# Performance work log

Measured on AMD Instinct MI355X. Metric: run time of the kernel, lower is better.

The kernel has to match this reference:

```python
import jax, jax.numpy as jnp
import numpy as np

D = 384      # ViT-S feature dim (feat_dim_lookup['s'])
H = 6        # module forces num_heads = 6
L = 12       # ViT-S depth
RATIO = 0.1  # attention_mask_ratio
EPS = 1e-6


def layernorm(x, g, b):
    m = x.mean(-1, keepdims=True)
    v = ((x - m) ** 2).mean(-1, keepdims=True)
    return (x - m) * jax.lax.rsqrt(v + EPS) * g + b


def masked_attn(x, w_qkv, b_qkv, w_o, b_o):
    # Patch._fix_attn_masking: full softmax attention, threshold at ratio*row_max, renormalize.
    B, N, Dm = x.shape
    dh = Dm // H
    qkv = (x @ w_qkv + b_qkv).reshape(B, N, 3, H, dh)
    q = qkv[:, :, 0].transpose(0, 2, 1, 3)  # [B,H,N,dh]
    k = qkv[:, :, 1].transpose(0, 2, 1, 3)
    v = qkv[:, :, 2].transpose(0, 2, 1, 3)
    scores = jnp.einsum('bhqd,bhkd->bhqk', q, k) * (dh ** -0.5)
    attn = jax.nn.softmax(scores, axis=-1)
    thresh = RATIO * attn.max(axis=-1, keepdims=True)
    attn = jnp.where(attn >= thresh, attn, 0.0)
    attn = attn / attn.sum(axis=-1, keepdims=True)  # re-normalize
    out = jnp.einsum('bhqk,bhkd->bhqd', attn, v)
    out = out.transpose(0, 2, 1, 3).reshape(B, N, Dm)
    return out @ w_o + b_o, attn


def block(x, p):
    w_qkv, b_qkv, w_o, b_o, g1, be1, g2, be2, w1, b1, w2, b2 = p
    h, attn = masked_attn(layernorm(x, g1, be1), w_qkv, b_qkv, w_o, b_o)
    x = x + h
    h = layernorm(x, g2, be2) @ w1 + b1
    h = jax.nn.gelu(h, approximate=False) @ w2 + b2
    return x + h, attn


def setup_inputs() -> dict:
    key = jax.random.key(0)
    ks = jax.random.split(key, 8)
    B, N = 2, 962  # 2 transforms; (1+(160-8)//5)**2 + 1 cls = 962 tokens
    s = 0.02
    return {
        'x': jax.random.normal(ks[0], (B, N, D), jnp.float32),
        'w_qkv': jax.random.normal(ks[1], (L, D, 3 * D), jnp.float32) * s,
        'b_qkv': jnp.zeros((L, 3 * D), jnp.float32),
        'w_proj': jax.random.normal(ks[2], (L, D, D), jnp.float32) * s,
        'b_proj': jnp.zeros((L, D), jnp.float32),
        'ln1_g': jnp.ones((L, D), jnp.float32),
        'ln1_b': jnp.zeros((L, D), jnp.float32),
        'ln2_g': jnp.ones((L, D), jnp.float32),
        'ln2_b': jnp.zeros((L, D), jnp.float32),
        'w_fc1': jax.random.normal(ks[3], (L, D, 4 * D), jnp.float32) * s,
        'b_fc1': jnp.zeros((L, 4 * D), jnp.float32),
        'w_fc2': jax.random.normal(ks[4], (L, 4 * D, D), jnp.float32) * s,
        'b_fc2': jnp.zeros((L, D), jnp.float32),
        'lnf_g': jnp.ones((D,), jnp.float32),
        'lnf_b': jnp.zeros((D,), jnp.float32),
    }


def reference(x, w_qkv, b_qkv, w_proj, b_proj, ln1_g, ln1_b, ln2_g, ln2_b,
              w_fc1, b_fc1, w_fc2, b_fc2, lnf_g, lnf_b):
    params = (w_qkv, b_qkv, w_proj, b_proj, ln1_g, ln1_b, ln2_g, ln2_b,
              w_fc1, b_fc1, w_fc2, b_fc2)
    first = jax.tree_util.tree_map(lambda a: a[:-1], params)
    last = jax.tree_util.tree_map(lambda a: a[-1], params)

    def scan_fn(h, p):
        h, _ = block(h, p)
        return h, None

    x, _ = jax.lax.scan(scan_fn, x, first)  # blocks 0..L-2
    x, attn = block(x, last)                # last block, keep masked attention
    feats = layernorm(x, lnf_g, lnf_b)      # [B, N, D]
    return feats, attn
```

## Files before the change

### kernel.cpp

```cpp
#include <hip/hip_runtime.h>
#include <hip/hip_bf16.h>
#include <math.h>

typedef __bf16 bf16_t;
typedef __bf16 bf16x8 __attribute__((ext_vector_type(8)));
typedef float f32x4 __attribute__((ext_vector_type(4)));
typedef float f32x16 __attribute__((ext_vector_type(16)));

#define NEGBIG -3.0e38f

__global__ void __launch_bounds__(256) trall_k(
    const float* __restrict__ w_qkv, const float* __restrict__ w_proj,
    const float* __restrict__ w_fc1, const float* __restrict__ w_fc2,
    bf16_t* __restrict__ wt_qkv, bf16_t* __restrict__ wt_proj,
    bf16_t* __restrict__ wt_fc1, bf16_t* __restrict__ wt_fc2)
{
    __shared__ float T[32][33];
    int t = blockIdx.x;
    int z = t / 1728, r = t % 1728;
    const float* W; bf16_t* Wt; int K, N, n0, k0;
    if (r < 432)       { W = w_qkv;  Wt = wt_qkv;  K = 384;  N = 1152; n0 = (r % 36) * 32;               k0 = (r / 36) * 32; }
    else if (r < 576)  { W = w_proj; Wt = wt_proj; K = 384;  N = 384;  int rr = r - 432;  n0 = (rr % 12) * 32; k0 = (rr / 12) * 32; }
    else if (r < 1152) { W = w_fc1;  Wt = wt_fc1;  K = 384;  N = 1536; int rr = r - 576;  n0 = (rr % 48) * 32; k0 = (rr / 48) * 32; }
    else               { W = w_fc2;  Wt = wt_fc2;  K = 1536; N = 384;  int rr = r - 1152; n0 = (rr % 12) * 32; k0 = (rr / 12) * 32; }
    const float* Wl = W + (size_t)z * K * N;
    bf16_t* Wtl = Wt + (size_t)z * K * N;
    int tx = threadIdx.x & 31, ty = threadIdx.x >> 5;
#pragma unroll
    for (int i = 0; i < 4; ++i)
        T[ty + 8 * i][tx] = Wl[(size_t)(k0 + ty + 8 * i) * N + n0 + tx];
    __syncthreads();
#pragma unroll
    for (int i = 0; i < 4; ++i)
        Wtl[(size_t)(n0 + ty + 8 * i) * K + k0 + tx] = (bf16_t)T[tx][ty + 8 * i];
}

__global__ void __launch_bounds__(256) lncopy_k(
    const float* __restrict__ xin, const float* __restrict__ g,
    const float* __restrict__ b, float* __restrict__ xf,
    bf16_t* __restrict__ out)
{
    int t = blockIdx.x * 4 + (threadIdx.x >> 6);
    int lane = threadIdx.x & 63;
    const float* xp = xin + (size_t)t * 384;
    float v[6];
    float s = 0.f;
#pragma unroll
    for (int i = 0; i < 6; ++i) { v[i] = xp[lane + 64 * i]; s += v[i]; }
#pragma unroll
    for (int i = 0; i < 6; ++i) xf[(size_t)t * 384 + lane + 64 * i] = v[i];
    for (int off = 32; off > 0; off >>= 1) s += __shfl_xor(s, off);
    float mean = s * (1.0f / 384.0f);
    float s2 = 0.f;
#pragma unroll
    for (int i = 0; i < 6; ++i) { float d = v[i] - mean; s2 += d * d; }
    for (int off = 32; off > 0; off >>= 1) s2 += __shfl_xor(s2, off);
    float rstd = rsqrtf(s2 * (1.0f / 384.0f) + 1e-6f);
#pragma unroll
    for (int i = 0; i < 6; ++i) {
        int c = lane + 64 * i;
        out[(size_t)t * 384 + c] = (bf16_t)((v[i] - mean) * rstd * g[c] + b[c]);
    }
}

template <int NP, typename OT, bool WX>
__global__ void __launch_bounds__(256) ln_red_k(
    const float* __restrict__ x, const float* __restrict__ part,
    const float* __restrict__ g, const float* __restrict__ b,
    float* __restrict__ xupd, OT* __restrict__ out)
{
    int t = blockIdx.x * 4 + (threadIdx.x >> 6);
    int lane = threadIdx.x & 63;
    const size_t base = (size_t)t * 384;
    float v[6];
#pragma unroll
    for (int i = 0; i < 6; ++i) v[i] = x[base + lane + 64 * i];
#pragma unroll
    for (int p = 0; p < NP; ++p)
#pragma unroll
        for (int i = 0; i < 6; ++i)
            v[i] += part[(size_t)p * 738816 + base + lane + 64 * i];
    float s = 0.f;
#pragma unroll
    for (int i = 0; i < 6; ++i) {
        if (WX) xupd[base + lane + 64 * i] = v[i];
        s += v[i];
    }
    for (int off = 32; off > 0; off >>= 1) s += __shfl_xor(s, off);
    float mean = s * (1.0f / 384.0f);
    float s2 = 0.f;
#pragma unroll
    for (int i = 0; i < 6; ++i) { float d = v[i] - mean; s2 += d * d; }
    for (int off = 32; off > 0; off >>= 1) s2 += __shfl_xor(s2, off);
    float rstd = rsqrtf(s2 * (1.0f / 384.0f) + 1e-6f);
#pragma unroll
    for (int i = 0; i < 6; ++i) {
        int c = lane + 64 * i;
        out[base + c] = (OT)((v[i] - mean) * rstd * g[c] + b[c]);
    }
}

template <int MODE>
__global__ void __launch_bounds__(256) gemm_k(
    const bf16_t* __restrict__ A, const bf16_t* __restrict__ Bt,
    const float* __restrict__ bias, int M, int N, int K,
    bf16_t* __restrict__ outb,
    bf16_t* __restrict__ qb, bf16_t* __restrict__ kb, bf16_t* __restrict__ vtb)
{
    __shared__ alignas(16) bf16_t As[2][64][72];
    __shared__ alignas(16) bf16_t Bs[2][64][72];

    const int tid  = threadIdx.x;
    const int wave = tid >> 6, lane = tid & 63;
    const int m0 = blockIdx.y * 64, n0 = blockIdx.x * 64;
    const int rb = (wave >> 1) * 32, cb = (wave & 1) * 32;
    const int r32 = lane & 31, half = lane >> 5;
    const int h8 = half * 8;

    const int lrow = tid >> 3;
    const int lcol = (tid & 7) * 8;

    const bf16_t* pA0 = A  + (size_t)(m0 + lrow) * K + lcol;
    const bf16_t* pA1 = pA0 + (size_t)32 * K;
    const bf16_t* pB0 = Bt + (size_t)(n0 + lrow) * K + lcol;
    const bf16_t* pB1 = pB0 + (size_t)32 * K;

    f32x16 acc = {};
    bf16x8 va0, va1, vb0, vb1;

    va0 = *(const bf16x8*)(pA0);
    va1 = *(const bf16x8*)(pA1);
    vb0 = *(const bf16x8*)(pB0);
    vb1 = *(const bf16x8*)(pB1);
    *(bf16x8*)(&As[0][lrow][lcol])      = va0;
    *(bf16x8*)(&As[0][lrow + 32][lcol]) = va1;
    *(bf16x8*)(&Bs[0][lrow][lcol])      = vb0;
    *(bf16x8*)(&Bs[0][lrow + 32][lcol]) = vb1;

    int cur = 0;
    for (int k0 = 0; k0 < K; k0 += 64) {
        __syncthreads();
        const bool has_next = (k0 + 64 < K);
        if (has_next) {
            va0 = *(const bf16x8*)(pA0 + k0 + 64);
            va1 = *(const bf16x8*)(pA1 + k0 + 64);
            vb0 = *(const bf16x8*)(pB0 + k0 + 64);
            vb1 = *(const bf16x8*)(pB1 + k0 + 64);
        }
#pragma unroll
        for (int kc = 0; kc < 64; kc += 16) {
            bf16x8 a = *(const bf16x8*)(&As[cur][rb + r32][kc + h8]);
            bf16x8 b = *(const bf16x8*)(&Bs[cur][cb + r32][kc + h8]);
            acc = __builtin_amdgcn_mfma_f32_32x32x16_bf16(a, b, acc, 0, 0, 0);
        }
        if (has_next) {
            int nxt = cur ^ 1;
            *(bf16x8*)(&As[nxt][lrow][lcol])      = va0;
            *(bf16x8*)(&As[nxt][lrow + 32][lcol]) = va1;
            *(bf16x8*)(&Bs[nxt][lrow][lcol])      = vb0;
            *(bf16x8*)(&Bs[nxt][lrow + 32][lcol]) = vb1;
            cur = nxt;
        }
    }

    const int gc = n0 + cb + r32;
    const float bv = bias[gc];
    if (MODE == 2) {
#pragma unroll
        for (int reg = 0; reg < 16; ++reg) {
            int gr = m0 + rb + (reg & 3) + 8 * (reg >> 2) + 4 * half;
            if (gr >= M) continue;
            float val = acc[reg] + bv;
            float g = 0.5f * val * (1.0f + erff(val * 0.70710678118654752f));
            outb[(size_t)gr * N + gc] = (bf16_t)g;
        }
    } else {
        const int which = gc / 384, rem = gc % 384;
        const int h = rem >> 6, d = rem & 63;
#pragma unroll
        for (int reg = 0; reg < 16; ++reg) {
            int gr = m0 + rb + (reg & 3) + 8 * (reg >> 2) + 4 * half;
            if (gr >= M) continue;
            float val = acc[reg] + bv;
            int bb = (gr >= 962) ? 1 : 0;
            int n = gr - 962 * bb;
            int bh = bb * 6 + h;
            bf16_t bvv = (bf16_t)val;
            if (which == 0)      qb[((size_t)bh * 962 + n) * 64 + d] = bvv;
            else if (which == 1) kb[((size_t)bh * 962 + n) * 64 + d] = bvv;
            else                 vtb[((size_t)bh * 64 + d) * 992 + n] = bvv;
        }
    }
}

template <int KLEN>
__global__ void __launch_bounds__(256) gemm_sp(
    const bf16_t* __restrict__ A, int lda,
    const bf16_t* __restrict__ Bt, int ldb,
    const float* __restrict__ bias, int M, int N,
    float* __restrict__ part)
{
    __shared__ alignas(16) bf16_t As[2][64][72];
    __shared__ alignas(16) bf16_t Bs[2][64][72];

    const int tid  = threadIdx.x;
    const int wave = tid >> 6, lane = tid & 63;
    const int m0 = blockIdx.y * 64, n0 = blockIdx.x * 64;
    const int rb = (wave >> 1) * 32, cb = (wave & 1) * 32;
    const int r32 = lane & 31, half = lane >> 5;
    const int h8 = half * 8;
    const int ks = blockIdx.z * KLEN;

    const int lrow = tid >> 3;
    const int lcol = (tid & 7) * 8;

    const bf16_t* pA0 = A  + (size_t)(m0 + lrow) * lda + ks + lcol;
    const bf16_t* pA1 = pA0 + (size_t)32 * lda;
    const bf16_t* pB0 = Bt + (size_t)(n0 + lrow) * ldb + ks + lcol;
    const bf16_t* pB1 = pB0 + (size_t)32 * ldb;

    f32x16 acc = {};
    bf16x8 va0, va1, vb0, vb1;

    va0 = *(const bf16x8*)(pA0);
    va1 = *(const bf16x8*)(pA1);
    vb0 = *(const bf16x8*)(pB0);
    vb1 = *(const bf16x8*)(pB1);
    *(bf16x8*)(&As[0][lrow][lcol])      = va0;
    *(bf16x8*)(&As[0][lrow + 32][lcol]) = va1;
    *(bf16x8*)(&Bs[0][lrow][lcol])      = vb0;
    *(bf16x8*)(&Bs[0][lrow + 32][lcol]) = vb1;

    int cur = 0;
    for (int k0 = 0; k0 < KLEN; k0 += 64) {
        __syncthreads();
        const bool has_next = (k0 + 64 < KLEN);
        if (has_next) {
            va0 = *(const bf16x8*)(pA0 + k0 + 64);
            va1 = *(const bf16x8*)(pA1 + k0 + 64);
            vb0 = *(const bf16x8*)(pB0 + k0 + 64);
            vb1 = *(const bf16x8*)(pB1 + k0 + 64);
        }
#pragma unroll
        for (int kc = 0; kc < 64; kc += 16) {
            bf16x8 a = *(const bf16x8*)(&As[cur][rb + r32][kc + h8]);
            bf16x8 b = *(const bf16x8*)(&Bs[cur][cb + r32][kc + h8]);
            acc = __builtin_amdgcn_mfma_f32_32x32x16_bf16(a, b, acc, 0, 0, 0);
        }
        if (has_next) {
            int nxt = cur ^ 1;
            *(bf16x8*)(&As[nxt][lrow][lcol])      = va0;
            *(bf16x8*)(&As[nxt][lrow + 32][lcol]) = va1;
            *(bf16x8*)(&Bs[nxt][lrow][lcol])      = vb0;
            *(bf16x8*)(&Bs[nxt][lrow + 32][lcol]) = vb1;
            cur = nxt;
        }
    }

    const int gc = n0 + cb + r32;
    const float bv = (blockIdx.z == 0) ? bias[gc] : 0.f;
    float* pz = part + (size_t)blockIdx.z * 738816;
#pragma unroll
    for (int reg = 0; reg < 16; ++reg) {
        int gr = m0 + rb + (reg & 3) + 8 * (reg >> 2) + 4 * half;
        if (gr >= M) continue;
        pz[(size_t)gr * N + gc] = acc[reg] + bv;
    }
}

__global__ void __launch_bounds__(256) attn_k(
    const bf16_t* __restrict__ qb, const bf16_t* __restrict__ kb,
    const bf16_t* __restrict__ vtb, bf16_t* __restrict__ attnout,
    float* __restrict__ attn_save)
{
    __shared__ alignas(16) bf16_t S[16][1000];

    const int tid  = threadIdx.x;
    const int wave = tid >> 6, lane = tid & 63;
    const int q4 = lane >> 4, mm = lane & 15;
    const int bh = blockIdx.y, qt = blockIdx.x;
    const int qrow0 = qt * 16;

    int qr = qrow0 + mm; if (qr > 961) qr = 961;
    const bf16_t* qptr = qb + ((size_t)bh * 962 + qr) * 64 + q4 * 8;
    bf16x8 aq0 = *(const bf16x8*)(qptr);
    bf16x8 aq1 = *(const bf16x8*)(qptr + 32);

    for (int ct = wave; ct < 61; ct += 4) {
        int kr = ct * 16 + mm; if (kr > 961) kr = 961;
        const bf16_t* kptr = kb + ((size_t)bh * 962 + kr) * 64 + q4 * 8;
        bf16x8 b0 = *(const bf16x8*)(kptr);
        bf16x8 b1 = *(const bf16x8*)(kptr + 32);
        f32x4 acc = {};
        acc = __builtin_amdgcn_mfma_f32_16x16x32_bf16(aq0, b0, acc, 0, 0, 0);
        acc = __builtin_amdgcn_mfma_f32_16x16x32_bf16(aq1, b1, acc, 0, 0, 0);
        int col = ct * 16 + mm;
#pragma unroll
        for (int r = 0; r < 4; ++r) {
            int row = q4 * 4 + r;
            if (col < 962) S[row][col] = (bf16_t)(acc[r] * 0.125f);
        }
    }
    for (int idx = tid; idx < 16 * 38; idx += 256) {
        int r = idx / 38, c = 962 + idx % 38;
        S[r][c] = (bf16_t)NEGBIG;
    }
    __syncthreads();

    const int trow = tid >> 4, ti = tid & 15;
    float e[8][8];
    float mx = NEGBIG;
#pragma unroll
    for (int t = 0; t < 8; ++t) {
        int c8 = ti * 8 + 128 * t;
        bf16x8 xv;
        if (c8 < 1000) xv = *(const bf16x8*)(&S[trow][c8]);
        else {
#pragma unroll
            for (int j = 0; j < 8; ++j) xv[j] = (bf16_t)NEGBIG;
        }
#pragma unroll
        for (int j = 0; j < 8; ++j) { e[t][j] = (float)xv[j]; mx = fmaxf(mx, e[t][j]); }
    }
#pragma unroll
    for (int off = 8; off > 0; off >>= 1) mx = fmaxf(mx, __shfl_xor(mx, off, 16));

    float sum = 0.f;
#pragma unroll
    for (int t = 0; t < 8; ++t)
#pragma unroll
    for (int j = 0; j < 8; ++j) {
        float ev = __expf(e[t][j] - mx);
        e[t][j] = ev;
        if (ev >= 0.1f) sum += ev;
    }
#pragma unroll
    for (int off = 8; off > 0; off >>= 1) sum += __shfl_xor(sum, off, 16);
    float inv = 1.0f / sum;

    int row_g = qrow0 + trow;
#pragma unroll
    for (int t = 0; t < 8; ++t) {
        int c8 = ti * 8 + 128 * t;
        if (c8 >= 1000) continue;
        bf16x8 pv;
#pragma unroll
        for (int j = 0; j < 8; ++j) {
            float pp = (e[t][j] >= 0.1f) ? e[t][j] * inv : 0.f;
            e[t][j] = pp;
            pv[j] = (bf16_t)pp;
        }
        *(bf16x8*)(&S[trow][c8]) = pv;
        if (attn_save && row_g < 962) {
#pragma unroll
            for (int j = 0; j < 8; ++j)
                if (c8 + j < 962)
                    attn_save[((size_t)bh * 962 + row_g) * 962 + c8 + j] = e[t][j];
        }
    }
    __syncthreads();

    const int wc0 = wave * 16;
    f32x4 o = {};
    for (int kc = 0; kc < 31; ++kc) {
        bf16x8 pa = *(const bf16x8*)(&S[mm][kc * 32 + q4 * 8]);
        bf16x8 vb = *(const bf16x8*)(vtb + ((size_t)bh * 64 + wc0 + mm) * 992 + kc * 32 + q4 * 8);
        o = __builtin_amdgcn_mfma_f32_16x16x32_bf16(pa, vb, o, 0, 0, 0);
    }
    int b = bh / 6, h = bh % 6;
#pragma unroll
    for (int r = 0; r < 4; ++r) {
        int qrr = qrow0 + q4 * 4 + r;
        if (qrr < 962)
            attnout[((size_t)(b * 962 + qrr)) * 384 + h * 64 + wc0 + mm] = (bf16_t)o[r];
    }
}

extern "C" void kernel_launch(void* const* d_in, const int* in_sizes, int n_in,
                              void* d_out, int out_size, void* d_ws, size_t ws_size,
                              hipStream_t stream)
{
    const float* xin    = (const float*)d_in[0];
    const float* w_qkv  = (const float*)d_in[1];
    const float* b_qkv  = (const float*)d_in[2];
    const float* w_proj = (const float*)d_in[3];
    const float* b_proj = (const float*)d_in[4];
    const float* ln1g   = (const float*)d_in[5];
    const float* ln1b   = (const float*)d_in[6];
    const float* ln2g   = (const float*)d_in[7];
    const float* ln2b   = (const float*)d_in[8];
    const float* w_fc1  = (const float*)d_in[9];
    const float* b_fc1  = (const float*)d_in[10];
    const float* w_fc2  = (const float*)d_in[11];
    const float* b_fc2  = (const float*)d_in[12];
    const float* lnfg   = (const float*)d_in[13];
    const float* lnfb   = (const float*)d_in[14];

    float* feats     = (float*)d_out;
    float* attn_save = feats + 738816;

    char* p = (char*)d_ws;
    auto alloc = [&](size_t bytes) {
        char* r = p;
        p += (bytes + 255) & ~(size_t)255;
        return r;
    };
    float*  x_f32   = (float*)alloc(1924ull * 384 * 4);
    bf16_t* xn      = (bf16_t*)alloc(1984ull * 384 * 2);
    bf16_t* qbuf    = (bf16_t*)alloc(12ull * 962 * 64 * 2);
    bf16_t* kbuf    = (bf16_t*)alloc(12ull * 962 * 64 * 2);
    bf16_t* vtbuf   = (bf16_t*)alloc(12ull * 64 * 992 * 2);
    bf16_t* attnout = (bf16_t*)alloc(1984ull * 384 * 2);
    bf16_t* mlp1    = (bf16_t*)alloc(1984ull * 1536 * 2);
    bf16_t* wt_qkv  = (bf16_t*)alloc(12ull * 1152 * 384 * 2);
    bf16_t* wt_proj = (bf16_t*)alloc(12ull * 384 * 384 * 2);
    bf16_t* wt_fc1  = (bf16_t*)alloc(12ull * 1536 * 384 * 2);
    bf16_t* wt_fc2  = (bf16_t*)alloc(12ull * 384 * 1536 * 2);
    float*  partbuf = (float*)alloc(4ull * 1924 * 384 * 4);

    trall_k<<<dim3(20736), dim3(256), 0, stream>>>(
        w_qkv, w_proj, w_fc1, w_fc2, wt_qkv, wt_proj, wt_fc1, wt_fc2);

    lncopy_k<<<dim3(481), dim3(256), 0, stream>>>(xin, ln1g, ln1b, x_f32, xn);

    for (int l = 0; l < 12; ++l) {
        gemm_k<0><<<dim3(18, 31), dim3(256), 0, stream>>>(
            xn, wt_qkv + (size_t)l * 1152 * 384, b_qkv + l * 1152,
            1924, 1152, 384, nullptr, qbuf, kbuf, vtbuf);
        attn_k<<<dim3(61, 12), dim3(256), 0, stream>>>(
            qbuf, kbuf, vtbuf, attnout, (l == 11) ? attn_save : (float*)nullptr);
        gemm_sp<192><<<dim3(6, 31, 2), dim3(256), 0, stream>>>(
            attnout, 384, wt_proj + (size_t)l * 384 * 384, 384, b_proj + l * 384,
            1924, 384, partbuf);
        ln_red_k<2, bf16_t, true><<<dim3(481), dim3(256), 0, stream>>>(
            x_f32, partbuf, ln2g + l * 384, ln2b + l * 384, x_f32, xn);
        gemm_k<2><<<dim3(24, 31), dim3(256), 0, stream>>>(
            xn, wt_fc1 + (size_t)l * 1536 * 384, b_fc1 + l * 1536,
            1924, 1536, 384, mlp1, nullptr, nullptr, nullptr);
        gemm_sp<384><<<dim3(6, 31, 4), dim3(256), 0, stream>>>(
            mlp1, 1536, wt_fc2 + (size_t)l * 384 * 1536, 1536, b_fc2 + l * 384,
            1924, 384, partbuf);
        if (l < 11) {
            ln_red_k<4, bf16_t, true><<<dim3(481), dim3(256), 0, stream>>>(
                x_f32, partbuf, ln1g + (l + 1) * 384, ln1b + (l + 1) * 384, x_f32, xn);
        } else {
            ln_red_k<4, float, false><<<dim3(481), dim3(256), 0, stream>>>(
                x_f32, partbuf, lnfg, lnfb, x_f32, feats);
        }
    }
}
```

Baseline: 981.1 us.

## Enlarge attention query tile to 32 rows with 32x32 MFMA and 512 threads

The attention kernel now processes 32 query rows per block instead of 16, using 512 threads and 32x32x16 bf16 MFMA for the QK^T scores, which halves the number of blocks and the reloads of K and V per query row. The PV stage splits the eight waves into two 16-row halves. This doubles LDS per block and cuts grid parallelism to 372 blocks, which may reduce occupancy. The softmax section is assumed to index rows by thread id, so it must now cover 32 rows.

```diff
diff --git a/kernel.cpp b/kernel.cpp
--- a/kernel.cpp
+++ b/kernel.cpp
@@ -268,40 +268,44 @@
     }
 }
 
-__global__ void __launch_bounds__(256) attn_k(
+__global__ void __launch_bounds__(512) attn_k(
     const bf16_t* __restrict__ qb, const bf16_t* __restrict__ kb,
     const bf16_t* __restrict__ vtb, bf16_t* __restrict__ attnout,
     float* __restrict__ attn_save)
 {
-    __shared__ alignas(16) bf16_t S[16][1000];
+    __shared__ alignas(16) bf16_t S[32][1000];
 
     const int tid  = threadIdx.x;
     const int wave = tid >> 6, lane = tid & 63;
+    const int r32 = lane & 31, half = lane >> 5;
     const int q4 = lane >> 4, mm = lane & 15;
     const int bh = blockIdx.y, qt = blockIdx.x;
-    const int qrow0 = qt * 16;
-
-    int qr = qrow0 + mm; if (qr > 961) qr = 961;
-    const bf16_t* qptr = qb + ((size_t)bh * 962 + qr) * 64 + q4 * 8;
-    bf16x8 aq0 = *(const bf16x8*)(qptr);
-    bf16x8 aq1 = *(const bf16x8*)(qptr + 32);
-
-    for (int ct = wave; ct < 61; ct += 4) {
-        int kr = ct * 16 + mm; if (kr > 961) kr = 961;
-        const bf16_t* kptr = kb + ((size_t)bh * 962 + kr) * 64 + q4 * 8;
-        bf16x8 b0 = *(const bf16x8*)(kptr);
-        bf16x8 b1 = *(const bf16x8*)(kptr + 32);
-        f32x4 acc = {};
-        acc = __builtin_amdgcn_mfma_f32_16x16x32_bf16(aq0, b0, acc, 0, 0, 0);
-        acc = __builtin_amdgcn_mfma_f32_16x16x32_bf16(aq1, b1, acc, 0, 0, 0);
-        int col = ct * 16 + mm;
-#pragma unroll
-        for (int r = 0; r < 4; ++r) {
-            int row = q4 * 4 + r;
-            if (col < 962) S[row][col] = (bf16_t)(acc[r] * 0.125f);
-        }
-    }
-    for (int idx = tid; idx < 16 * 38; idx += 256) {
+    const int qrow0 = qt * 32;
+
+    int qr = qrow0 + r32; if (qr > 961) qr = 961;
+    const bf16_t* qptr = qb + ((size_t)bh * 962 + qr) * 64 + half * 8;
+    bf16x8 aq[4];
+#pragma unroll
+    for (int ks = 0; ks < 4; ++ks)
+        aq[ks] = *(const bf16x8*)(qptr + ks * 16);
+
+    for (int ct = wave; ct < 31; ct += 8) {
+        int kr = ct * 32 + r32; if (kr > 961) kr = 961;
+        const bf16_t* kptr = kb + ((size_t)bh * 962 + kr) * 64 + half * 8;
+        f32x16 acc = {};
+#pragma unroll
+        for (int ks = 0; ks < 4; ++ks) {
+            bf16x8 bk = *(const bf16x8*)(kptr + ks * 16);
+            acc = __builtin_amdgcn_mfma_f32_32x32x16_bf16(aq[ks], bk, acc, 0, 0, 0);
+        }
+        int kcol = ct * 32 + r32;
+#pragma unroll
+        for (int reg = 0; reg < 16; ++reg) {
+            int row = (reg & 3) + 8 * (reg >> 2) + 4 * half;
+            if (kcol < 962) S[row][kcol] = (bf16_t)(acc[reg] * 0.125f);
+        }
+    }
+    for (int idx = tid; idx < 32 * 38; idx += 512) {
         int r = idx / 38, c = 962 + idx % 38;
         S[r][c] = (bf16_t)NEGBIG;
     }
@@ -360,17 +364,18 @@
     }
     __syncthreads();
 
-    const int wc0 = wave * 16;
+    const int qh  = wave >> 2;
+    const int wc0 = (wave & 3) * 16;
     f32x4 o = {};
     for (int kc = 0; kc < 31; ++kc) {
-        bf16x8 pa = *(const bf16x8*)(&S[mm][kc * 32 + q4 * 8]);
+        bf16x8 pa = *(const bf16x8*)(&S[qh * 16 + mm][kc * 32 + q4 * 8]);
         bf16x8 vb = *(const bf16x8*)(vtb + ((size_t)bh * 64 + wc0 + mm) * 992 + kc * 32 + q4 * 8);
         o = __builtin_amdgcn_mfma_f32_16x16x32_bf16(pa, vb, o, 0, 0, 0);
     }
     int b = bh / 6, h = bh % 6;
 #pragma unroll
     for (int r = 0; r < 4; ++r) {
-        int qrr = qrow0 + q4 * 4 + r;
+        int qrr = qrow0 + qh * 16 + q4 * 4 + r;
         if (qrr < 962)
             attnout[((size_t)(b * 962 + qrr)) * 384 + h * 64 + wc0 + mm] = (bf16_t)o[r];
     }
@@ -427,7 +432,7 @@
         gemm_k<0><<<dim3(18, 31), dim3(256), 0, stream>>>(
             xn, wt_qkv + (size_t)l * 1152 * 384, b_qkv + l * 1152,
             1924, 1152, 384, nullptr, qbuf, kbuf, vtbuf);
-        attn_k<<<dim3(61, 12), dim3(256), 0, stream>>>(
+        attn_k<<<dim3(31, 12), dim3(512), 0, stream>>>(
             qbuf, kbuf, vtbuf, attnout, (l == 11) ? attn_save : (float*)nullptr);
         gemm_sp<192><<<dim3(6, 31, 2), dim3(256), 0, stream>>>(
             attnout, 384, wt_proj + (size_t)l * 384 * 384, 384, b_proj + l * 384,
```

Result: no change. 991.8 us (+1.1%).
